# Kernel optimization log

Measured on AMD Instinct MI355X. Metric: run time of the kernel, lower is better.

Reference implementation:

```python
import jax, jax.numpy as jnp
import numpy as np

N_NODES = 50000
N_EDGES = 800000
D_IN = 128
D_OUT = 128


def setup_inputs() -> dict:
    key = jax.random.key(0)
    k1, k2, k3, k4, k5 = jax.random.split(key, 5)
    # xavier-uniform-like scale for the two linear layers (gain for relu ~ sqrt(2))
    bound = float(np.sqrt(2.0) * np.sqrt(6.0 / (D_IN + D_OUT)))
    return {
        "feat": jax.random.normal(k1, (N_NODES, D_IN), dtype=jnp.float32),
        "w_neigh": jax.random.uniform(k2, (D_OUT, D_IN), minval=-bound, maxval=bound, dtype=jnp.float32),
        "w_self": jax.random.uniform(k3, (D_OUT, D_IN), minval=-bound, maxval=bound, dtype=jnp.float32),
        "b_self": jnp.zeros((D_OUT,), dtype=jnp.float32),
        "rows": jax.random.randint(k4, (N_EDGES,), 0, N_NODES, dtype=jnp.int32),  # src node per edge
        "cols": jax.random.randint(k5, (N_EDGES,), 0, N_NODES, dtype=jnp.int32),  # dst node per edge
    }


def reference(feat, w_neigh, w_self, b_self, rows, cols):
    n = feat.shape[0]
    # srcdata = fc_neigh(feat): [N, D_OUT]
    srcdata = feat @ w_neigh.T
    # deg[j] = A.sum(0)[j] = in-degree of destination j (column sums)
    deg = jax.ops.segment_sum(jnp.ones_like(cols, dtype=feat.dtype), cols, num_segments=n)
    # dstdata = (A @ diag(deg)^-1).T @ srcdata  ==  mean over incoming src neighbors
    agg = jax.ops.segment_sum(srcdata[rows], cols, num_segments=n)  # [N, D_OUT]
    dstdata = agg / jnp.where(deg > 0, deg, 1.0)[:, None]
    # rst = fc_self(h_self) + dstdata
    return feat @ w_self.T + b_self + dstdata
```

## Files before the change

### kernel.cpp

```cpp
#include <hip/hip_runtime.h>
#include <hip/hip_bf16.h>

#define D 128
#define CAP 64
#define TILE 32

typedef __attribute__((ext_vector_type(8))) short bf16x8;
typedef __attribute__((ext_vector_type(4))) float floatx4;
typedef __attribute__((ext_vector_type(2))) float floatx2;

__device__ __forceinline__ unsigned short f2bf(float f) {
    unsigned int u = __float_as_uint(f);
    return (unsigned short)((u + 0x7fffu + ((u >> 16) & 1u)) >> 16);
}

__global__ __launch_bounds__(256) void zero_kernel(int* __restrict__ p, int n) {
    int i = blockIdx.x * 256 + threadIdx.x;
    if (i < n) p[i] = 0;
}

__global__ __launch_bounds__(256) void prep_fill_kernel(
    const float* __restrict__ feat,
    const float* __restrict__ w_self,
    const float* __restrict__ w_neigh,
    const int* __restrict__ rows,
    const int* __restrict__ cols,
    unsigned short* __restrict__ feat_h,
    unsigned int* __restrict__ feat_q,
    unsigned short* __restrict__ ws_h,
    unsigned short* __restrict__ wn_h,
    int* __restrict__ cursor,
    unsigned short* __restrict__ slots,
    int n_nodes, int n_edges)
{
    const int b = blockIdx.x;
    const int tid = threadIdx.x;
    const int role = b % 3;

    if (role < 2) {
        int pb = (b / 3) * 2 + role;
        int i  = pb * 256 + tid;
        if (i < n_nodes * 32) {
            float4 v = *(const float4*)&feat[(long long)4 * i];
            ushort4 o;
            o.x = f2bf(v.x); o.y = f2bf(v.y); o.z = f2bf(v.z); o.w = f2bf(v.w);
            *(ushort4*)&feat_h[(long long)4 * i] = o;
            int q = __builtin_amdgcn_cvt_pk_fp8_f32(v.x, v.y, 0, false);
            q = __builtin_amdgcn_cvt_pk_fp8_f32(v.z, v.w, q, true);
            feat_q[i] = (unsigned int)q;
        }
    } else {
        int fb = b / 3;
        int e  = fb * 256 + tid;
        if (e < n_edges) {
            int c = cols[e];
            int p = atomicAdd(&cursor[c], 1);
            if (p < CAP) slots[c * CAP + p] = (unsigned short)rows[e];
        }
        if (fb < 32) {
            int i = fb * 256 + tid;
            int j = i & 4095;
            const float* src = (i < 4096) ? w_self : w_neigh;
            unsigned short* dst = (i < 4096) ? ws_h : wn_h;
            float4 v = *(const float4*)&src[4 * j];
            ushort4 o;
            o.x = f2bf(v.x); o.y = f2bf(v.y); o.z = f2bf(v.z); o.w = f2bf(v.w);
            *(ushort4*)&dst[4 * j] = o;
        }
    }
}

__global__ __launch_bounds__(256, 4) void agg_gemm_kernel(
    const unsigned short* __restrict__ feat_h,
    const unsigned int* __restrict__ feat_q,
    const int* __restrict__ cursor,
    const unsigned short* __restrict__ slots,
    const unsigned short* __restrict__ ws_h,
    const unsigned short* __restrict__ wn_h,
    const float* __restrict__ b_self,
    float* __restrict__ out,
    int n_nodes)
{
    __shared__ unsigned short s_agg[TILE][136];

    const int tid  = threadIdx.x;
    const int row0 = blockIdx.x * TILE;

    {
        const int ln   = tid & 7;
        const int nl   = tid >> 3;
        const int node = row0 + nl;

        float acc[16];
        #pragma unroll
        for (int i = 0; i < 16; ++i) acc[i] = 0.f;

        if (node < n_nodes) {
            int deg = cursor[node];
            if (deg > CAP) deg = CAP;
            const unsigned short* slotp = slots + (long long)node * CAP;

            for (int k0 = 0; k0 < deg; k0 += 8) {
                uint4 sc = *(const uint4*)(slotp + k0);
                unsigned int sv[4] = {sc.x, sc.y, sc.z, sc.w};
                int cnt = deg - k0; if (cnt > 8) cnt = 8;

                uint4 g[8];
                #pragma unroll
                for (int j = 0; j < 8; ++j) {
                    if (j < cnt) {
                        int r = (int)((sv[j >> 1] >> ((j & 1) * 16)) & 0xffffu);
                        g[j] = *(const uint4*)(feat_q + (long long)r * 32 + ln * 4);
                    }
                }
                #pragma unroll
                for (int j = 0; j < 8; ++j) {
                    if (j < cnt) {
                        unsigned int w[4] = {g[j].x, g[j].y, g[j].z, g[j].w};
                        #pragma unroll
                        for (int c = 0; c < 4; ++c) {
                            floatx2 lo = __builtin_amdgcn_cvt_pk_f32_fp8((int)w[c], false);
                            floatx2 hi = __builtin_amdgcn_cvt_pk_f32_fp8((int)w[c], true);
                            acc[c * 4 + 0] += lo.x;
                            acc[c * 4 + 1] += lo.y;
                            acc[c * 4 + 2] += hi.x;
                            acc[c * 4 + 3] += hi.y;
                        }
                    }
                }
            }
            float inv = (deg > 0) ? 1.0f / (float)deg : 0.0f;
            #pragma unroll
            for (int c = 0; c < 4; ++c) {
                ushort4 o;
                o.x = f2bf(acc[c * 4 + 0] * inv);
                o.y = f2bf(acc[c * 4 + 1] * inv);
                o.z = f2bf(acc[c * 4 + 2] * inv);
                o.w = f2bf(acc[c * 4 + 3] * inv);
                *(ushort4*)&s_agg[nl][ln * 16 + c * 4] = o;
            }
        } else {
            #pragma unroll
            for (int c = 0; c < 4; ++c)
                *(ushort4*)&s_agg[nl][ln * 16 + c * 4] = (ushort4){0, 0, 0, 0};
        }
    }
    __syncthreads();

    const int wave  = tid >> 6;
    const int lane  = tid & 63;
    const int m     = lane & 15;
    const int quad  = lane >> 4;
    const int kq    = quad * 8;
    const int rsub  = (wave & 1) * 16;
    const int rbase = row0 + rsub;
    const int cbase = (wave >> 1) * 64;

    floatx4 gacc[4];
    #pragma unroll
    for (int nt = 0; nt < 4; ++nt) gacc[nt] = (floatx4){0.f, 0.f, 0.f, 0.f};

    int rA = rbase + m;
    if (rA > n_nodes - 1) rA = n_nodes - 1;

    #pragma unroll
    for (int kt = 0; kt < 4; ++kt) {
        const int k = kt * 32 + kq;
        bf16x8 a = *(const bf16x8*)&feat_h[(long long)rA * D + k];
        #pragma unroll
        for (int nt = 0; nt < 4; ++nt) {
            bf16x8 b = *(const bf16x8*)&ws_h[(cbase + nt * 16 + m) * D + k];
            gacc[nt] = __builtin_amdgcn_mfma_f32_16x16x32_bf16(a, b, gacc[nt], 0, 0, 0);
        }
    }
    #pragma unroll
    for (int kt = 0; kt < 4; ++kt) {
        const int k = kt * 32 + kq;
        bf16x8 a = *(const bf16x8*)&s_agg[rsub + m][k];
        #pragma unroll
        for (int nt = 0; nt < 4; ++nt) {
            bf16x8 b = *(const bf16x8*)&wn_h[(cbase + nt * 16 + m) * D + k];
            gacc[nt] = __builtin_amdgcn_mfma_f32_16x16x32_bf16(a, b, gacc[nt], 0, 0, 0);
        }
    }

    #pragma unroll
    for (int nt = 0; nt < 4; ++nt) {
        int col = cbase + nt * 16 + m;
        float bias = b_self[col];
        #pragma unroll
        for (int r = 0; r < 4; ++r) {
            int row = rbase + quad * 4 + r;
            if (row < n_nodes)
                out[(long long)row * D + col] = gacc[nt][r] + bias;
        }
    }
}

extern "C" void kernel_launch(void* const* d_in, const int* in_sizes, int n_in,
                              void* d_out, int out_size, void* d_ws, size_t ws_size,
                              hipStream_t stream) {
    const float* feat    = (const float*)d_in[0];
    const float* w_neigh = (const float*)d_in[1];
    const float* w_self  = (const float*)d_in[2];
    const float* b_self  = (const float*)d_in[3];
    const int*   rows    = (const int*)d_in[4];
    const int*   cols    = (const int*)d_in[5];
    float* out = (float*)d_out;

    const int n_nodes = in_sizes[0] / D;
    const int n_edges = in_sizes[4];

    unsigned short* feat_h = (unsigned short*)d_ws;
    unsigned int*   feat_q = (unsigned int*)(feat_h + (size_t)n_nodes * D);
    unsigned short* slots  = (unsigned short*)(feat_q + (size_t)n_nodes * 32);
    int* cursor = (int*)(slots + (size_t)n_nodes * CAP);
    unsigned short* ws_h = (unsigned short*)(cursor + n_nodes);
    unsigned short* wn_h = ws_h + 16384;

    zero_kernel<<<(n_nodes + 255) / 256, 256, 0, stream>>>(cursor, n_nodes);

    int nblocks = (n_nodes * 32 + 255) / 256 + (n_edges + 255) / 256;
    prep_fill_kernel<<<nblocks, 256, 0, stream>>>(
        feat, w_self, w_neigh, rows, cols,
        feat_h, feat_q, ws_h, wn_h, cursor, slots, n_nodes, n_edges);

    agg_gemm_kernel<<<(n_nodes + TILE - 1) / TILE, 256, 0, stream>>>(
        feat_h, feat_q, cursor, slots, ws_h, wn_h, b_self, out, n_nodes);
}
```

Before: 188.2 us.

## Balance neighbor gather across tile via chunk work list and drop bf16 feat copy

The aggregation phase now builds a per-tile list of 8-edge chunks so all 32 thread groups share the gather work evenly instead of one group per node. Partial sums are combined with shared-memory float atomics before the mean and bf16 conversion. Separately, the bf16 copy of feat is no longer written in the prep kernel; the GEMM reads fp32 feat directly and converts in registers, removing a write and a read of an intermediate buffer. The cost is extra shared memory (a 16KB accumulator), more barriers, LDS atomics, and twice the bytes read for the self-term A operand.

```diff
diff --git a/kernel.cpp b/kernel.cpp
--- a/kernel.cpp
+++ b/kernel.cpp
@@ -25,7 +25,6 @@
     const float* __restrict__ w_neigh,
     const int* __restrict__ rows,
     const int* __restrict__ cols,
-    unsigned short* __restrict__ feat_h,
     unsigned int* __restrict__ feat_q,
     unsigned short* __restrict__ ws_h,
     unsigned short* __restrict__ wn_h,
@@ -42,9 +41,6 @@
         int i  = pb * 256 + tid;
         if (i < n_nodes * 32) {
             float4 v = *(const float4*)&feat[(long long)4 * i];
-            ushort4 o;
-            o.x = f2bf(v.x); o.y = f2bf(v.y); o.z = f2bf(v.z); o.w = f2bf(v.w);
-            *(ushort4*)&feat_h[(long long)4 * i] = o;
             int q = __builtin_amdgcn_cvt_pk_fp8_f32(v.x, v.y, 0, false);
             q = __builtin_amdgcn_cvt_pk_fp8_f32(v.z, v.w, q, true);
             feat_q[i] = (unsigned int)q;
@@ -71,7 +67,7 @@
 }
 
 __global__ __launch_bounds__(256, 4) void agg_gemm_kernel(
-    const unsigned short* __restrict__ feat_h,
+    const float* __restrict__ feat,
     const unsigned int* __restrict__ feat_q,
     const int* __restrict__ cursor,
     const unsigned short* __restrict__ slots,
@@ -81,68 +77,109 @@
     float* __restrict__ out,
     int n_nodes)
 {
+    __shared__ float s_acc[TILE][D];
     __shared__ unsigned short s_agg[TILE][136];
+    __shared__ unsigned short s_work[TILE * 8];
+    __shared__ int s_deg[TILE];
+    __shared__ int s_total;
 
     const int tid  = threadIdx.x;
     const int row0 = blockIdx.x * TILE;
 
+    if (tid < TILE) {
+        int node = row0 + tid;
+        int d = 0;
+        if (node < n_nodes) {
+            d = cursor[node];
+            if (d > CAP) d = CAP;
+        }
+        s_deg[tid] = d;
+    }
+    __syncthreads();
+
+    if (tid < TILE) {
+        int pre = 0;
+        #pragma unroll 8
+        for (int j = 0; j < TILE; ++j) {
+            int cj = (s_deg[j] + 7) >> 3;
+            if (j < tid) pre += cj;
+        }
+        int my = (s_deg[tid] + 7) >> 3;
+        for (int c = 0; c < my; ++c)
+            s_work[pre + c] = (unsigned short)((tid << 3) | c);
+        if (tid == TILE - 1) s_total = pre + my;
+    }
     {
-        const int ln   = tid & 7;
-        const int nl   = tid >> 3;
-        const int node = row0 + nl;
-
-        float acc[16];
-        #pragma unroll
-        for (int i = 0; i < 16; ++i) acc[i] = 0.f;
-
-        if (node < n_nodes) {
-            int deg = cursor[node];
-            if (deg > CAP) deg = CAP;
-            const unsigned short* slotp = slots + (long long)node * CAP;
-
-            for (int k0 = 0; k0 < deg; k0 += 8) {
-                uint4 sc = *(const uint4*)(slotp + k0);
-                unsigned int sv[4] = {sc.x, sc.y, sc.z, sc.w};
-                int cnt = deg - k0; if (cnt > 8) cnt = 8;
-
-                uint4 g[8];
-                #pragma unroll
-                for (int j = 0; j < 8; ++j) {
-                    if (j < cnt) {
-                        int r = (int)((sv[j >> 1] >> ((j & 1) * 16)) & 0xffffu);
-                        g[j] = *(const uint4*)(feat_q + (long long)r * 32 + ln * 4);
-                    }
+        float4 z = make_float4(0.f, 0.f, 0.f, 0.f);
+        float* p = &s_acc[0][0] + tid * 16;
+        *(float4*)(p + 0) = z; *(float4*)(p + 4) = z;
+        *(float4*)(p + 8) = z; *(float4*)(p + 12) = z;
+    }
+    __syncthreads();
+
+    {
+        const int g  = tid >> 3;
+        const int ln = tid & 7;
+        const int total = s_total;
+
+        for (int u = g; u < total; u += 32) {
+            int w     = s_work[u];
+            int nl    = w >> 3;
+            int k0    = (w & 7) * 8;
+            int deg   = s_deg[nl];
+            int cnt   = deg - k0; if (cnt > 8) cnt = 8;
+
+            const unsigned short* slotp = slots + (long long)(row0 + nl) * CAP;
+            uint4 sc = *(const uint4*)(slotp + k0);
+            unsigned int sv[4] = {sc.x, sc.y, sc.z, sc.w};
+
+            uint4 gbuf[8];
+            #pragma unroll
+            for (int j = 0; j < 8; ++j) {
+                if (j < cnt) {
+                    int r = (int)((sv[j >> 1] >> ((j & 1) * 16)) & 0xffffu);
+                    gbuf[j] = *(const uint4*)(feat_q + (long long)r * 32 + ln * 4);
                 }
-                #pragma unroll
-                for (int j = 0; j < 8; ++j) {
-                    if (j < cnt) {
-                        unsigned int w[4] = {g[j].x, g[j].y, g[j].z, g[j].w};
-                        #pragma unroll
-                        for (int c = 0; c < 4; ++c) {
-                            floatx2 lo = __builtin_amdgcn_cvt_pk_f32_fp8((int)w[c], false);
-                            floatx2 hi = __builtin_amdgcn_cvt_pk_f32_fp8((int)w[c], true);
-                            acc[c * 4 + 0] += lo.x;
-                            acc[c * 4 + 1] += lo.y;
-                            acc[c * 4 + 2] += hi.x;
-                            acc[c * 4 + 3] += hi.y;
-                        }
+            }
+            float acc[16];
+            #pragma unroll
+            for (int i = 0; i < 16; ++i) acc[i] = 0.f;
+            #pragma unroll
+            for (int j = 0; j < 8; ++j) {
+                if (j < cnt) {
+                    unsigned int wv[4] = {gbuf[j].x, gbuf[j].y, gbuf[j].z, gbuf[j].w};
+                    #pragma unroll
+                    for (int c = 0; c < 4; ++c) {
+                        floatx2 lo = __builtin_amdgcn_cvt_pk_f32_fp8((int)wv[c], false);
+                        floatx2 hi = __builtin_amdgcn_cvt_pk_f32_fp8((int)wv[c], true);
+                        acc[c * 4 + 0] += lo.x;
+                        acc[c * 4 + 1] += lo.y;
+                        acc[c * 4 + 2] += hi.x;
+                        acc[c * 4 + 3] += hi.y;
                     }
                 }
             }
-            float inv = (deg > 0) ? 1.0f / (float)deg : 0.0f;
-            #pragma unroll
-            for (int c = 0; c < 4; ++c) {
-                ushort4 o;
-                o.x = f2bf(acc[c * 4 + 0] * inv);
-                o.y = f2bf(acc[c * 4 + 1] * inv);
-                o.z = f2bf(acc[c * 4 + 2] * inv);
-                o.w = f2bf(acc[c * 4 + 3] * inv);
-                *(ushort4*)&s_agg[nl][ln * 16 + c * 4] = o;
-            }
-        } else {
-            #pragma unroll
-            for (int c = 0; c < 4; ++c)
-                *(ushort4*)&s_agg[nl][ln * 16 + c * 4] = (ushort4){0, 0, 0, 0};
+            float* dst = &s_acc[nl][ln * 16];
+            #pragma unroll
+            for (int i = 0; i < 16; ++i) atomicAdd(&dst[i], acc[i]);
+        }
+    }
+    __syncthreads();
+
+    {
+        const int nl = tid >> 3;
+        const int ln = tid & 7;
+        int deg = s_deg[nl];
+        float inv = (deg > 0) ? 1.0f / (float)deg : 0.0f;
+        const float* src = &s_acc[nl][ln * 16];
+        #pragma unroll
+        for (int c = 0; c < 4; ++c) {
+            ushort4 o;
+            o.x = f2bf(src[c * 4 + 0] * inv);
+            o.y = f2bf(src[c * 4 + 1] * inv);
+            o.z = f2bf(src[c * 4 + 2] * inv);
+            o.w = f2bf(src[c * 4 + 3] * inv);
+            *(ushort4*)&s_agg[nl][ln * 16 + c * 4] = o;
         }
     }
     __syncthreads();
@@ -166,7 +203,13 @@
     #pragma unroll
     for (int kt = 0; kt < 4; ++kt) {
         const int k = kt * 32 + kq;
-        bf16x8 a = *(const bf16x8*)&feat_h[(long long)rA * D + k];
+        float4 f0 = *(const float4*)&feat[(long long)rA * D + k];
+        float4 f1 = *(const float4*)&feat[(long long)rA * D + k + 4];
+        bf16x8 a;
+        a[0] = (short)f2bf(f0.x); a[1] = (short)f2bf(f0.y);
+        a[2] = (short)f2bf(f0.z); a[3] = (short)f2bf(f0.w);
+        a[4] = (short)f2bf(f1.x); a[5] = (short)f2bf(f1.y);
+        a[6] = (short)f2bf(f1.z); a[7] = (short)f2bf(f1.w);
         #pragma unroll
         for (int nt = 0; nt < 4; ++nt) {
             bf16x8 b = *(const bf16x8*)&ws_h[(cbase + nt * 16 + m) * D + k];
@@ -211,8 +254,7 @@
     const int n_nodes = in_sizes[0] / D;
     const int n_edges = in_sizes[4];
 
-    unsigned short* feat_h = (unsigned short*)d_ws;
-    unsigned int*   feat_q = (unsigned int*)(feat_h + (size_t)n_nodes * D);
+    unsigned int*   feat_q = (unsigned int*)d_ws;
     unsigned short* slots  = (unsigned short*)(feat_q + (size_t)n_nodes * 32);
     int* cursor = (int*)(slots + (size_t)n_nodes * CAP);
     unsigned short* ws_h = (unsigned short*)(cursor + n_nodes);
@@ -223,8 +265,8 @@
     int nblocks = (n_nodes * 32 + 255) / 256 + (n_edges + 255) / 256;
     prep_fill_kernel<<<nblocks, 256, 0, stream>>>(
         feat, w_self, w_neigh, rows, cols,
-        feat_h, feat_q, ws_h, wn_h, cursor, slots, n_nodes, n_edges);
+        feat_q, ws_h, wn_h, cursor, slots, n_nodes, n_edges);
 
     agg_gemm_kernel<<<(n_nodes + TILE - 1) / TILE, 256, 0, stream>>>(
-        feat_h, feat_q, cursor, slots, ws_h, wn_h, b_self, out, n_nodes);
-}
+        feat, feat_q, cursor, slots, ws_h, wn_h, b_self, out, n_nodes);
+}
```

After: 240.0 us. 27.5% more time.

## Drop bf16 feature copy, halve node tile, split neighbor gather across lane pairs

Applied to the files above, without the earlier changes.

The prep kernel no longer writes a bf16 copy of the features. The fused kernel instead reads fp32 features and converts them to bf16 in registers for the self GEMM, which removes a full write and read of the feature array. The tile is reduced to 16 nodes per block with 16 threads per node; each pair of lanes splits the neighbor list and combines partial sums with a shuffle, raising gather parallelism and block count. The self GEMM is now issued before the barrier so it can overlap the aggregation. The cost is a larger fp32 read of feat in the GEMM and more blocks, each re-reading the weights.

```diff
diff --git a/kernel.cpp b/kernel.cpp
--- a/kernel.cpp
+++ b/kernel.cpp
@@ -3,7 +3,7 @@
 
 #define D 128
 #define CAP 64
-#define TILE 32
+#define TILE 16
 
 typedef __attribute__((ext_vector_type(8))) short bf16x8;
 typedef __attribute__((ext_vector_type(4))) float floatx4;
@@ -25,7 +25,6 @@
     const float* __restrict__ w_neigh,
     const int* __restrict__ rows,
     const int* __restrict__ cols,
-    unsigned short* __restrict__ feat_h,
     unsigned int* __restrict__ feat_q,
     unsigned short* __restrict__ ws_h,
     unsigned short* __restrict__ wn_h,
@@ -42,9 +41,6 @@
         int i  = pb * 256 + tid;
         if (i < n_nodes * 32) {
             float4 v = *(const float4*)&feat[(long long)4 * i];
-            ushort4 o;
-            o.x = f2bf(v.x); o.y = f2bf(v.y); o.z = f2bf(v.z); o.w = f2bf(v.w);
-            *(ushort4*)&feat_h[(long long)4 * i] = o;
             int q = __builtin_amdgcn_cvt_pk_fp8_f32(v.x, v.y, 0, false);
             q = __builtin_amdgcn_cvt_pk_fp8_f32(v.z, v.w, q, true);
             feat_q[i] = (unsigned int)q;
@@ -70,8 +66,8 @@
     }
 }
 
-__global__ __launch_bounds__(256, 4) void agg_gemm_kernel(
-    const unsigned short* __restrict__ feat_h,
+__global__ __launch_bounds__(256, 6) void agg_gemm_kernel(
+    const float* __restrict__ feat,
     const unsigned int* __restrict__ feat_q,
     const int* __restrict__ cursor,
     const unsigned short* __restrict__ slots,
@@ -82,53 +78,72 @@
     int n_nodes)
 {
     __shared__ unsigned short s_agg[TILE][136];
+    __shared__ int s_deg[TILE];
 
     const int tid  = threadIdx.x;
     const int row0 = blockIdx.x * TILE;
 
+    if (tid < TILE) {
+        int node = row0 + tid;
+        int d = 0;
+        if (node < n_nodes) {
+            d = cursor[node];
+            if (d > CAP) d = CAP;
+        }
+        s_deg[tid] = d;
+    }
+    __syncthreads();
+
     {
-        const int ln   = tid & 7;
-        const int nl   = tid >> 3;
-        const int node = row0 + nl;
+        const int nl  = tid >> 4;
+        const int t16 = tid & 15;
+        const int sub = t16 & 1;
+        const int ln  = t16 >> 1;
+        const int deg = s_deg[nl];
 
         float acc[16];
         #pragma unroll
         for (int i = 0; i < 16; ++i) acc[i] = 0.f;
 
-        if (node < n_nodes) {
-            int deg = cursor[node];
-            if (deg > CAP) deg = CAP;
-            const unsigned short* slotp = slots + (long long)node * CAP;
-
-            for (int k0 = 0; k0 < deg; k0 += 8) {
-                uint4 sc = *(const uint4*)(slotp + k0);
-                unsigned int sv[4] = {sc.x, sc.y, sc.z, sc.w};
-                int cnt = deg - k0; if (cnt > 8) cnt = 8;
-
-                uint4 g[8];
-                #pragma unroll
-                for (int j = 0; j < 8; ++j) {
-                    if (j < cnt) {
-                        int r = (int)((sv[j >> 1] >> ((j & 1) * 16)) & 0xffffu);
-                        g[j] = *(const uint4*)(feat_q + (long long)r * 32 + ln * 4);
-                    }
+        const unsigned short* slotp = slots + (long long)(row0 + nl) * CAP;
+
+        for (int k0 = 0; k0 < deg; k0 += 16) {
+            uint4 s0 = *(const uint4*)(slotp + k0);
+            uint4 s1 = *(const uint4*)(slotp + k0 + 8);
+            unsigned int sv[8] = {s0.x, s0.y, s0.z, s0.w, s1.x, s1.y, s1.z, s1.w};
+            int cnt = deg - k0; if (cnt > 16) cnt = 16;
+
+            uint4 g[8];
+            #pragma unroll
+            for (int jj = 0; jj < 8; ++jj) {
+                int j = jj * 2 + sub;
+                if (j < cnt) {
+                    int r = (int)((sv[j >> 1] >> ((j & 1) * 16)) & 0xffffu);
+                    g[jj] = *(const uint4*)(feat_q + (long long)r * 32 + ln * 4);
                 }
-                #pragma unroll
-                for (int j = 0; j < 8; ++j) {
-                    if (j < cnt) {
-                        unsigned int w[4] = {g[j].x, g[j].y, g[j].z, g[j].w};
-                        #pragma unroll
-                        for (int c = 0; c < 4; ++c) {
-                            floatx2 lo = __builtin_amdgcn_cvt_pk_f32_fp8((int)w[c], false);
-                            floatx2 hi = __builtin_amdgcn_cvt_pk_f32_fp8((int)w[c], true);
-                            acc[c * 4 + 0] += lo.x;
-                            acc[c * 4 + 1] += lo.y;
-                            acc[c * 4 + 2] += hi.x;
-                            acc[c * 4 + 3] += hi.y;
-                        }
+            }
+            #pragma unroll
+            for (int jj = 0; jj < 8; ++jj) {
+                int j = jj * 2 + sub;
+                if (j < cnt) {
+                    unsigned int wv[4] = {g[jj].x, g[jj].y, g[jj].z, g[jj].w};
+                    #pragma unroll
+                    for (int c = 0; c < 4; ++c) {
+                        floatx2 lo = __builtin_amdgcn_cvt_pk_f32_fp8((int)wv[c], false);
+                        floatx2 hi = __builtin_amdgcn_cvt_pk_f32_fp8((int)wv[c], true);
+                        acc[c * 4 + 0] += lo.x;
+                        acc[c * 4 + 1] += lo.y;
+                        acc[c * 4 + 2] += hi.x;
+                        acc[c * 4 + 3] += hi.y;
                     }
                 }
             }
+        }
+
+        #pragma unroll
+        for (int i = 0; i < 16; ++i) acc[i] += __shfl_xor(acc[i], 1);
+
+        if (sub == 0) {
             float inv = (deg > 0) ? 1.0f / (float)deg : 0.0f;
             #pragma unroll
             for (int c = 0; c < 4; ++c) {
@@ -139,58 +154,60 @@
                 o.w = f2bf(acc[c * 4 + 3] * inv);
                 *(ushort4*)&s_agg[nl][ln * 16 + c * 4] = o;
             }
-        } else {
-            #pragma unroll
-            for (int c = 0; c < 4; ++c)
-                *(ushort4*)&s_agg[nl][ln * 16 + c * 4] = (ushort4){0, 0, 0, 0};
-        }
-    }
-    __syncthreads();
+        }
+    }
 
     const int wave  = tid >> 6;
     const int lane  = tid & 63;
     const int m     = lane & 15;
     const int quad  = lane >> 4;
     const int kq    = quad * 8;
-    const int rsub  = (wave & 1) * 16;
-    const int rbase = row0 + rsub;
-    const int cbase = (wave >> 1) * 64;
-
-    floatx4 gacc[4];
-    #pragma unroll
-    for (int nt = 0; nt < 4; ++nt) gacc[nt] = (floatx4){0.f, 0.f, 0.f, 0.f};
-
-    int rA = rbase + m;
+    const int cbase = wave * 32;
+
+    floatx4 gacc[2];
+    gacc[0] = (floatx4){0.f, 0.f, 0.f, 0.f};
+    gacc[1] = (floatx4){0.f, 0.f, 0.f, 0.f};
+
+    int rA = row0 + m;
     if (rA > n_nodes - 1) rA = n_nodes - 1;
 
     #pragma unroll
     for (int kt = 0; kt < 4; ++kt) {
         const int k = kt * 32 + kq;
-        bf16x8 a = *(const bf16x8*)&feat_h[(long long)rA * D + k];
-        #pragma unroll
-        for (int nt = 0; nt < 4; ++nt) {
+        float4 f0 = *(const float4*)&feat[(long long)rA * D + k];
+        float4 f1 = *(const float4*)&feat[(long long)rA * D + k + 4];
+        bf16x8 a;
+        a[0] = (short)f2bf(f0.x); a[1] = (short)f2bf(f0.y);
+        a[2] = (short)f2bf(f0.z); a[3] = (short)f2bf(f0.w);
+        a[4] = (short)f2bf(f1.x); a[5] = (short)f2bf(f1.y);
+        a[6] = (short)f2bf(f1.z); a[7] = (short)f2bf(f1.w);
+        #pragma unroll
+        for (int nt = 0; nt < 2; ++nt) {
             bf16x8 b = *(const bf16x8*)&ws_h[(cbase + nt * 16 + m) * D + k];
             gacc[nt] = __builtin_amdgcn_mfma_f32_16x16x32_bf16(a, b, gacc[nt], 0, 0, 0);
         }
     }
+
+    __syncthreads();
+
     #pragma unroll
     for (int kt = 0; kt < 4; ++kt) {
         const int k = kt * 32 + kq;
-        bf16x8 a = *(const bf16x8*)&s_agg[rsub + m][k];
-        #pragma unroll
-        for (int nt = 0; nt < 4; ++nt) {
+        bf16x8 a = *(const bf16x8*)&s_agg[m][k];
+        #pragma unroll
+        for (int nt = 0; nt < 2; ++nt) {
             bf16x8 b = *(const bf16x8*)&wn_h[(cbase + nt * 16 + m) * D + k];
             gacc[nt] = __builtin_amdgcn_mfma_f32_16x16x32_bf16(a, b, gacc[nt], 0, 0, 0);
         }
     }
 
     #pragma unroll
-    for (int nt = 0; nt < 4; ++nt) {
+    for (int nt = 0; nt < 2; ++nt) {
         int col = cbase + nt * 16 + m;
         float bias = b_self[col];
         #pragma unroll
         for (int r = 0; r < 4; ++r) {
-            int row = rbase + quad * 4 + r;
+            int row = row0 + quad * 4 + r;
             if (row < n_nodes)
                 out[(long long)row * D + col] = gacc[nt][r] + bias;
         }
@@ -211,8 +228,7 @@
     const int n_nodes = in_sizes[0] / D;
     const int n_edges = in_sizes[4];
 
-    unsigned short* feat_h = (unsigned short*)d_ws;
-    unsigned int*   feat_q = (unsigned int*)(feat_h + (size_t)n_nodes * D);
+    unsigned int*   feat_q = (unsigned int*)d_ws;
     unsigned short* slots  = (unsigned short*)(feat_q + (size_t)n_nodes * 32);
     int* cursor = (int*)(slots + (size_t)n_nodes * CAP);
     unsigned short* ws_h = (unsigned short*)(cursor + n_nodes);
@@ -223,8 +239,8 @@
     int nblocks = (n_nodes * 32 + 255) / 256 + (n_edges + 255) / 256;
     prep_fill_kernel<<<nblocks, 256, 0, stream>>>(
         feat, w_self, w_neigh, rows, cols,
-        feat_h, feat_q, ws_h, wn_h, cursor, slots, n_nodes, n_edges);
+        feat_q, ws_h, wn_h, cursor, slots, n_nodes, n_edges);
 
     agg_gemm_kernel<<<(n_nodes + TILE - 1) / TILE, 256, 0, stream>>>(
-        feat_h, feat_q, cursor, slots, ws_h, wn_h, b_self, out, n_nodes);
-}
+        feat, feat_q, cursor, slots, ws_h, wn_h, b_self, out, n_nodes);
+}
```

Measured after the change: 181.1 us. 3.8% less time.
